# Kernel optimization log

Measured on AMD Instinct MI355X. Metric: run time of the kernel, lower is better.

The kernel has to match this reference:

```python
import jax, jax.numpy as jnp
import numpy as np

N_HEADS = 2

def setup_inputs() -> dict:
    key = jax.random.key(0)
    ks = jax.random.split(key, 10)
    d, bank, b, t = 192, 1000, 16, 4096
    s = 1.0 / np.sqrt(d)
    return {
        "z": jax.random.normal(ks[0], (b, d, t), jnp.float32),
        "memory_bank": jax.random.normal(ks[1], (d, bank), jnp.float32),
        "Wq": jax.random.normal(ks[2], (d, d), jnp.float32) * s,
        "bq": jax.random.normal(ks[3], (d,), jnp.float32) * 0.02,
        "Wk": jax.random.normal(ks[4], (d, d), jnp.float32) * s,
        "bk": jax.random.normal(ks[5], (d,), jnp.float32) * 0.02,
        "Wv": jax.random.normal(ks[6], (d, d), jnp.float32) * s,
        "bv": jax.random.normal(ks[7], (d,), jnp.float32) * 0.02,
        "Wo": jax.random.normal(ks[8], (d, d), jnp.float32) * s,
        "bo": jax.random.normal(ks[9], (d,), jnp.float32) * 0.02,
    }


def _split_heads(x):
    # x: [b, d, t] -> [b, h, t, dk]  (matches view(b, h, dk, t).transpose(2, 3))
    b, d, t = x.shape
    dk = d // N_HEADS
    return x.reshape(b, N_HEADS, dk, t).transpose(0, 1, 3, 2)


def reference(z, memory_bank, Wq, bq, Wk, bk, Wv, bv, Wo, bo):
    b, d, t = z.shape
    dk = d // N_HEADS
    # memory bank expanded over batch: [b, d, bank]
    c = jnp.broadcast_to(memory_bank[None], (b,) + memory_bank.shape)
    # 1x1 conv projections == per-channel linear
    q = jnp.einsum('oc,bct->bot', Wq, z) + bq[None, :, None]
    k = jnp.einsum('oc,bcs->bos', Wk, c) + bk[None, :, None]
    v = jnp.einsum('oc,bcs->bos', Wv, c) + bv[None, :, None]
    qh = _split_heads(q)  # [b, h, t, dk]
    kh = _split_heads(k)  # [b, h, bank, dk]
    vh = _split_heads(v)  # [b, h, bank, dk]
    scores = jnp.einsum('bhtd,bhsd->bhts', qh, kh) / jnp.sqrt(jnp.asarray(dk, z.dtype))
    p = jax.nn.softmax(scores, axis=-1)  # [b, h, t, bank]
    out = jnp.einsum('bhts,bhsd->bhtd', p, vh)  # [b, h, t, dk]
    out = out.transpose(0, 1, 3, 2).reshape(b, d, t)  # merge heads -> [b, d, t]
    return jnp.einsum('oc,bct->bot', Wo, out) + bo[None, :, None]
```

## Files before the change

### kernel.cpp

```cpp
#include <hip/hip_runtime.h>


typedef float  f32x4  __attribute__((ext_vector_type(4)));
typedef __bf16 bf16;
typedef __bf16 bf16x4 __attribute__((ext_vector_type(4)));
typedef __bf16 bf16x8 __attribute__((ext_vector_type(8)));

#define B_   16
#define D_   192
#define T_   4096
#define BANK 1000
#define SP   1024
#define DK   96
#define SCALE 0.10206207261596577f
#define LOG2E 1.4426950408889634f

__global__ __launch_bounds__(256) void kv_kernel(
    const float* __restrict__ mb, const float* __restrict__ Wk, const float* __restrict__ bk,
    const float* __restrict__ Wv, const float* __restrict__ bv,
    bf16* __restrict__ ktg, bf16* __restrict__ vtg) {
  int s = blockIdx.x * 256 + threadIdx.x;
  int o = blockIdx.y;
  int h = o / DK, i = o % DK;
  float ak = 0.f, av = 0.f;
  if (s < BANK) {
    ak = bk[o]; av = bv[o];
    for (int c = 0; c < D_; ++c) {
      float m = mb[c * BANK + s];
      ak += Wk[o * D_ + c] * m;
      av += Wv[o * D_ + c] * m;
    }
  }
  ktg[(size_t)(h * SP + s) * DK + i] = (bf16)ak;
  vtg[(size_t)(h * DK + i) * SP + s] = (bf16)av;
}

__global__ __launch_bounds__(256) void proj_kernel(
    const bf16* __restrict__ XT, const float* __restrict__ W,
    const float* __restrict__ bias, float* __restrict__ Y) {
  __shared__ __align__(16) char smem[24576];
  bf16* sB = (bf16*)smem;
  float* sE = (float*)smem;

  const int tid = threadIdx.x;
  const int t0 = blockIdx.x * 256, o0 = blockIdx.y * 64, b = blockIdx.z;
  const int lane = tid & 63, wv = tid >> 6;
  const int quad = lane >> 4, l15 = lane & 15;

  const bf16* ap[4];
#pragma unroll
  for (int m = 0; m < 4; ++m)
    ap[m] = &XT[((size_t)b * T_ + t0 + (wv * 4 + m) * 16 + l15) * D_ + quad * 8];
  bf16x8 acur[4];
#pragma unroll
  for (int m = 0; m < 4; ++m) acur[m] = *(const bf16x8*)ap[m];

#pragma unroll
  for (int r = 0; r < 6; ++r) {
    int g = tid + 256 * r;
    int kb = g >> 8, nt = (g >> 6) & 3, qd = (g >> 4) & 3, l5 = g & 15;
    const float* wp = &W[(o0 + nt * 16 + l5) * D_ + kb * 32 + qd * 8];
    f32x4 wa = *(const f32x4*)wp, wb = *(const f32x4*)(wp + 4);
    bf16x8 pk;
#pragma unroll
    for (int u = 0; u < 4; ++u) { pk[u] = (bf16)wa[u]; pk[4 + u] = (bf16)wb[u]; }
    *(bf16x8*)&sB[(size_t)g * 8] = pk;
  }

  f32x4 acc[4][4];
#pragma unroll
  for (int m = 0; m < 4; ++m)
#pragma unroll
    for (int n = 0; n < 4; ++n) acc[m][n] = (f32x4){0.f, 0.f, 0.f, 0.f};

  __syncthreads();
  for (int kb = 0; kb < 6; ++kb) {
    bf16x8 anext[4];
    if (kb < 5) {
#pragma unroll
      for (int m = 0; m < 4; ++m)
        anext[m] = *(const bf16x8*)(ap[m] + (kb + 1) * 32);
    }
    bf16x8 bf[4];
#pragma unroll
    for (int n = 0; n < 4; ++n)
      bf[n] = *(const bf16x8*)&sB[(size_t)((kb * 4 + n) * 64 + lane) * 8];
#pragma unroll
    for (int m = 0; m < 4; ++m)
#pragma unroll
      for (int n = 0; n < 4; ++n)
        acc[m][n] = __builtin_amdgcn_mfma_f32_16x16x32_bf16(acur[m], bf[n], acc[m][n], 0, 0, 0);
    if (kb < 5) {
#pragma unroll
      for (int m = 0; m < 4; ++m) acur[m] = anext[m];
    }
  }
  __syncthreads();

  float bs[4];
#pragma unroll
  for (int n = 0; n < 4; ++n) bs[n] = bias[o0 + n * 16 + l15];
  float* se = sE + wv * 1088;
#pragma unroll
  for (int m = 0; m < 4; ++m) {
#pragma unroll
    for (int n = 0; n < 4; ++n)
#pragma unroll
      for (int r = 0; r < 4; ++r)
        se[(quad * 4 + r) * 68 + n * 16 + l15] = acc[m][n][r] + bs[n];
#pragma unroll
    for (int p = 0; p < 4; ++p) {
      int o = p * 16 + (lane >> 2), tq = (lane & 3) * 4;
      f32x4 vv;
#pragma unroll
      for (int u = 0; u < 4; ++u) vv[u] = se[(tq + u) * 68 + o];
      *(f32x4*)&Y[((size_t)b * D_ + o0 + o) * T_ + t0 + wv * 64 + m * 16 + tq] = vv;
    }
  }
}

__global__ __launch_bounds__(512) void attn_kernel(
    const float* __restrict__ z, const float* __restrict__ Wq,
    const float* __restrict__ bq, const bf16* __restrict__ ktg,
    const bf16* __restrict__ vtg, bf16* __restrict__ owsT) {
  __shared__ __align__(16) char smem[32768];
  bf16* kt = (bf16*)smem;
  bf16* vt = (bf16*)(smem + 12288);
  bf16* sP = (bf16*)(smem + 24576);
  bf16* qt = (bf16*)smem;

  const int tid = threadIdx.x;
  const int t0 = blockIdx.x * 128, h = blockIdx.y, b = blockIdx.z;
  const int lane = tid & 63, wv = tid >> 6;
  const int quad = lane >> 4, l15 = lane & 15;

  const bf16* kb_g = ktg + (size_t)h * SP * DK;
  const bf16* vb_g = vtg + (size_t)h * DK * SP;
  const bf16* sp_ptr[3];
  int sp_str[3];
#pragma unroll
  for (int r = 0; r < 3; ++r) {
    int g = tid + 512 * r;
    if (g < 768) {
      int kb = g >> 8, n = (g >> 6) & 3, qd = (g >> 4) & 3, l5 = g & 15;
      sp_ptr[r] = kb_g + (size_t)(n * 16 + l5) * DK + kb * 32 + qd * 8;
      sp_str[r] = 64 * DK;
    } else {
      int gv = g - 768, blk = gv >> 6;
      int kbv = blk / 6, n = blk % 6, qd = (gv >> 4) & 3, l5 = gv & 15;
      sp_ptr[r] = vb_g + (size_t)(n * 16 + l5) * SP + kbv * 32 + qd * 8;
      sp_str[r] = 64;
    }
  }
  bf16x8 kreg[3];
#pragma unroll
  for (int r = 0; r < 3; ++r) kreg[r] = *(const bf16x8*)sp_ptr[r];

  f32x4 qacc[6];
#pragma unroll
  for (int n = 0; n < 6; ++n) qacc[n] = (f32x4){0.f, 0.f, 0.f, 0.f};
  const float* zcol = &z[((size_t)b * D_ + quad * 8) * T_ + t0 + wv * 16 + l15];
  const float* wrow = &Wq[(size_t)(h * DK + l15) * D_ + quad * 8];
  for (int kb = 0; kb < 6; ++kb) {
    bf16x8 zf;
#pragma unroll
    for (int j = 0; j < 8; ++j)
      zf[j] = (bf16)zcol[(size_t)(kb * 32 + j) * T_];
#pragma unroll
    for (int n = 0; n < 6; ++n) {
      const float* wp = wrow + (size_t)n * 16 * D_ + kb * 32;
      f32x4 wa = *(const f32x4*)wp, wb = *(const f32x4*)(wp + 4);
      bf16x8 wf;
#pragma unroll
      for (int u = 0; u < 4; ++u) { wf[u] = (bf16)wa[u]; wf[4 + u] = (bf16)wb[u]; }
      qacc[n] = __builtin_amdgcn_mfma_f32_16x16x32_bf16(wf, zf, qacc[n], 0, 0, 0);
    }
  }
#pragma unroll
  for (int n = 0; n < 6; ++n) {
    f32x4 bq4 = *(const f32x4*)&bq[h * DK + n * 16 + quad * 4];
    int g = ((n & 1) * 2 + (quad >> 1)) * 16 + l15;
    int gs = g ^ ((g >> 3) & 7);
    bf16x4 pk;
#pragma unroll
    for (int r = 0; r < 4; ++r)
      pk[r] = (bf16)((qacc[n][r] + bq4[r]) * (SCALE * LOG2E));
    *(bf16x4*)&qt[(size_t)(((n >> 1) * 8 + wv) * 64 + gs) * 8 + (quad & 1) * 4] = pk;
  }
  bf16x8 qf[3];
#pragma unroll
  for (int kb = 0; kb < 3; ++kb)
    qf[kb] = *(const bf16x8*)&qt[(size_t)((kb * 8 + wv) * 64 + (lane ^ ((lane >> 3) & 7))) * 8];

  f32x4 oaccT[6];
#pragma unroll
  for (int n = 0; n < 6; ++n) oaccT[n] = (f32x4){0.f, 0.f, 0.f, 0.f};
  float m_run = -1e30f, l_run = 0.f;

  for (int ch = 0; ch < 16; ++ch) {
    __syncthreads();
#pragma unroll
    for (int r = 0; r < 3; ++r)
      *(bf16x8*)(smem + (size_t)(tid + 512 * r) * 16) = kreg[r];
    __syncthreads();
    if (ch < 15) {
#pragma unroll
      for (int r = 0; r < 3; ++r) {
        sp_ptr[r] += sp_str[r];
        kreg[r] = *(const bf16x8*)sp_ptr[r];
      }
    }

    f32x4 scT[4];
#pragma unroll
    for (int n = 0; n < 4; ++n) scT[n] = (f32x4){0.f, 0.f, 0.f, 0.f};
#pragma unroll
    for (int kb = 0; kb < 3; ++kb) {
#pragma unroll
      for (int n = 0; n < 4; ++n) {
        bf16x8 kf = *(const bf16x8*)&kt[(size_t)((kb * 4 + n) * 64 + lane) * 8];
        scT[n] = __builtin_amdgcn_mfma_f32_16x16x32_bf16(kf, qf[kb], scT[n], 0, 0, 0);
      }
    }
    if (ch == 15) {
#pragma unroll
      for (int r = 0; r < 4; ++r) {
        scT[3][r] = -1e30f;
        if (quad >= 2) scT[2][r] = -1e30f;
      }
    }

    float m8[8];
#pragma unroll
    for (int u = 0; u < 8; ++u)
      m8[u] = fmaxf(scT[u >> 1][(u & 1) * 2], scT[u >> 1][(u & 1) * 2 + 1]);
    float m4a = fmaxf(m8[0], m8[1]), m4b = fmaxf(m8[2], m8[3]);
    float m4c = fmaxf(m8[4], m8[5]), m4d = fmaxf(m8[6], m8[7]);
    float m0 = fmaxf(fmaxf(m4a, m4b), fmaxf(m4c, m4d));
    m0 = fmaxf(m0, __shfl_xor(m0, 16, 64));
    m0 = fmaxf(m0, __shfl_xor(m0, 32, 64));
    if (!__all(m0 - m_run <= 8.f)) {
      float mn = fmaxf(m_run, m0);
      float al = exp2f(m_run - mn);
      m_run = mn;
      l_run *= al;
#pragma unroll
      for (int n = 0; n < 6; ++n)
#pragma unroll
        for (int r = 0; r < 4; ++r) oaccT[n][r] *= al;
    }
    float pr[4][4];
#pragma unroll
    for (int n = 0; n < 4; ++n)
#pragma unroll
      for (int r = 0; r < 4; ++r) pr[n][r] = exp2f(scT[n][r] - m_run);
    float s8[8];
#pragma unroll
    for (int u = 0; u < 8; ++u)
      s8[u] = pr[u >> 1][(u & 1) * 2] + pr[u >> 1][(u & 1) * 2 + 1];
    float s4a = s8[0] + s8[1], s4b = s8[2] + s8[3];
    float s4c = s8[4] + s8[5], s4d = s8[6] + s8[7];
    float ls = (s4a + s4b) + (s4c + s4d);
    ls += __shfl_xor(ls, 16, 64);
    ls += __shfl_xor(ls, 32, 64);
    l_run += ls;

#pragma unroll
    for (int kb2 = 0; kb2 < 2; ++kb2) {
#pragma unroll
      for (int nh = 0; nh < 2; ++nh) {
        int n = kb2 * 2 + nh;
        int g = (nh * 2 + (quad >> 1)) * 16 + l15;
        int gs = g ^ ((g >> 3) & 7);
        bf16x4 pk = {(bf16)pr[n][0], (bf16)pr[n][1], (bf16)pr[n][2], (bf16)pr[n][3]};
        *(bf16x4*)&sP[(size_t)(wv * 64 + gs) * 8 + (quad & 1) * 4] = pk;
      }
      bf16x8 pa = *(const bf16x8*)&sP[(size_t)(wv * 64 + (lane ^ ((lane >> 3) & 7))) * 8];
#pragma unroll
      for (int n2 = 0; n2 < 6; ++n2) {
        bf16x8 vf = *(const bf16x8*)&vt[(size_t)((kb2 * 6 + n2) * 64 + lane) * 8];
        oaccT[n2] = __builtin_amdgcn_mfma_f32_16x16x32_bf16(vf, pa, oaccT[n2], 0, 0, 0);
      }
    }
  }

  float inv = 1.0f / l_run;
  bf16* orow = &owsT[((size_t)b * T_ + t0 + wv * 16 + l15) * D_ + h * DK + quad * 4];
#pragma unroll
  for (int n2 = 0; n2 < 6; ++n2) {
    bf16x4 pk = {(bf16)(oaccT[n2][0] * inv), (bf16)(oaccT[n2][1] * inv),
                 (bf16)(oaccT[n2][2] * inv), (bf16)(oaccT[n2][3] * inv)};
    *(bf16x4*)&orow[n2 * 16] = pk;
  }
}

extern "C" void kernel_launch(void* const* d_in, const int* in_sizes, int n_in,
                              void* d_out, int out_size, void* d_ws, size_t ws_size,
                              hipStream_t stream) {
  const float* z  = (const float*)d_in[0];
  const float* mb = (const float*)d_in[1];
  const float* Wq = (const float*)d_in[2];
  const float* bq = (const float*)d_in[3];
  const float* Wk = (const float*)d_in[4];
  const float* bk = (const float*)d_in[5];
  const float* Wv = (const float*)d_in[6];
  const float* bv = (const float*)d_in[7];
  const float* Wo = (const float*)d_in[8];
  const float* bo = (const float*)d_in[9];
  float* out = (float*)d_out;

  bf16* ktg  = (bf16*)d_ws;
  bf16* vtg  = ktg + 2 * SP * DK;
  bf16* owsT = vtg + 2 * DK * SP;

  kv_kernel  <<<dim3(SP / 256, D_),    256, 0, stream>>>(mb, Wk, bk, Wv, bv, ktg, vtg);
  attn_kernel<<<dim3(T_ / 128, 2, B_), 512, 0, stream>>>(z, Wq, bq, ktg, vtg, owsT);
  proj_kernel<<<dim3(T_ / 256, 3, B_), 256, 0, stream>>>(owsT, Wo, bo, out);
}
```

Baseline: 257.2 us.

## Process two query tiles per wave in attention kernel with 256 threads

Halves the attention block to 4 waves, with each wave handling two 16-row query tiles instead of one. Each K/V fragment read from shared memory now feeds two MFMAs, which roughly halves LDS reads per unit of work. Each thread also stages twice as many K/V registers from global memory. The cost is higher register pressure (doubled accumulators, 6 prefetch registers) and fewer waves per block for hiding latency. Shared memory grows to 40 KB to hold per-tile P buffers.

```diff
diff --git a/kernel.cpp b/kernel.cpp
--- a/kernel.cpp
+++ b/kernel.cpp
@@ -119,11 +119,11 @@
   }
 }
 
-__global__ __launch_bounds__(512) void attn_kernel(
+__global__ __launch_bounds__(256) void attn_kernel(
     const float* __restrict__ z, const float* __restrict__ Wq,
     const float* __restrict__ bq, const bf16* __restrict__ ktg,
     const bf16* __restrict__ vtg, bf16* __restrict__ owsT) {
-  __shared__ __align__(16) char smem[32768];
+  __shared__ __align__(16) char smem[40960];
   bf16* kt = (bf16*)smem;
   bf16* vt = (bf16*)(smem + 12288);
   bf16* sP = (bf16*)(smem + 24576);
@@ -136,11 +136,11 @@
 
   const bf16* kb_g = ktg + (size_t)h * SP * DK;
   const bf16* vb_g = vtg + (size_t)h * DK * SP;
-  const bf16* sp_ptr[3];
-  int sp_str[3];
-#pragma unroll
-  for (int r = 0; r < 3; ++r) {
-    int g = tid + 512 * r;
+  const bf16* sp_ptr[6];
+  int sp_str[6];
+#pragma unroll
+  for (int r = 0; r < 6; ++r) {
+    int g = tid + 256 * r;
     if (g < 768) {
       int kb = g >> 8, n = (g >> 6) & 3, qd = (g >> 4) & 3, l5 = g & 15;
       sp_ptr[r] = kb_g + (size_t)(n * 16 + l5) * DK + kb * 32 + qd * 8;
@@ -152,20 +152,24 @@
       sp_str[r] = 64;
     }
   }
-  bf16x8 kreg[3];
-#pragma unroll
-  for (int r = 0; r < 3; ++r) kreg[r] = *(const bf16x8*)sp_ptr[r];
-
-  f32x4 qacc[6];
-#pragma unroll
-  for (int n = 0; n < 6; ++n) qacc[n] = (f32x4){0.f, 0.f, 0.f, 0.f};
-  const float* zcol = &z[((size_t)b * D_ + quad * 8) * T_ + t0 + wv * 16 + l15];
+  bf16x8 kreg[6];
+#pragma unroll
+  for (int r = 0; r < 6; ++r) kreg[r] = *(const bf16x8*)sp_ptr[r];
+
+  f32x4 qacc[2][6];
+#pragma unroll
+  for (int t2 = 0; t2 < 2; ++t2)
+#pragma unroll
+    for (int n = 0; n < 6; ++n) qacc[t2][n] = (f32x4){0.f, 0.f, 0.f, 0.f};
+  const float* zc0 = &z[((size_t)b * D_ + quad * 8) * T_ + t0 + wv * 32 + l15];
   const float* wrow = &Wq[(size_t)(h * DK + l15) * D_ + quad * 8];
   for (int kb = 0; kb < 6; ++kb) {
-    bf16x8 zf;
-#pragma unroll
-    for (int j = 0; j < 8; ++j)
-      zf[j] = (bf16)zcol[(size_t)(kb * 32 + j) * T_];
+    bf16x8 zf[2];
+#pragma unroll
+    for (int t2 = 0; t2 < 2; ++t2)
+#pragma unroll
+      for (int j = 0; j < 8; ++j)
+        zf[t2][j] = (bf16)zc0[(size_t)(kb * 32 + j) * T_ + t2 * 16];
 #pragma unroll
     for (int n = 0; n < 6; ++n) {
       const float* wp = wrow + (size_t)n * 16 * D_ + kb * 32;
@@ -173,124 +177,158 @@
       bf16x8 wf;
 #pragma unroll
       for (int u = 0; u < 4; ++u) { wf[u] = (bf16)wa[u]; wf[4 + u] = (bf16)wb[u]; }
-      qacc[n] = __builtin_amdgcn_mfma_f32_16x16x32_bf16(wf, zf, qacc[n], 0, 0, 0);
-    }
-  }
-#pragma unroll
-  for (int n = 0; n < 6; ++n) {
-    f32x4 bq4 = *(const f32x4*)&bq[h * DK + n * 16 + quad * 4];
-    int g = ((n & 1) * 2 + (quad >> 1)) * 16 + l15;
-    int gs = g ^ ((g >> 3) & 7);
-    bf16x4 pk;
-#pragma unroll
-    for (int r = 0; r < 4; ++r)
-      pk[r] = (bf16)((qacc[n][r] + bq4[r]) * (SCALE * LOG2E));
-    *(bf16x4*)&qt[(size_t)(((n >> 1) * 8 + wv) * 64 + gs) * 8 + (quad & 1) * 4] = pk;
-  }
-  bf16x8 qf[3];
-#pragma unroll
-  for (int kb = 0; kb < 3; ++kb)
-    qf[kb] = *(const bf16x8*)&qt[(size_t)((kb * 8 + wv) * 64 + (lane ^ ((lane >> 3) & 7))) * 8];
-
-  f32x4 oaccT[6];
-#pragma unroll
-  for (int n = 0; n < 6; ++n) oaccT[n] = (f32x4){0.f, 0.f, 0.f, 0.f};
-  float m_run = -1e30f, l_run = 0.f;
+      qacc[0][n] = __builtin_amdgcn_mfma_f32_16x16x32_bf16(wf, zf[0], qacc[0][n], 0, 0, 0);
+      qacc[1][n] = __builtin_amdgcn_mfma_f32_16x16x32_bf16(wf, zf[1], qacc[1][n], 0, 0, 0);
+    }
+  }
+#pragma unroll
+  for (int t2 = 0; t2 < 2; ++t2)
+#pragma unroll
+    for (int n = 0; n < 6; ++n) {
+      f32x4 bq4 = *(const f32x4*)&bq[h * DK + n * 16 + quad * 4];
+      int g = ((n & 1) * 2 + (quad >> 1)) * 16 + l15;
+      int gs = g ^ ((g >> 3) & 7);
+      bf16x4 pk;
+#pragma unroll
+      for (int r = 0; r < 4; ++r)
+        pk[r] = (bf16)((qacc[t2][n][r] + bq4[r]) * (SCALE * LOG2E));
+      *(bf16x4*)&qt[(size_t)(((n >> 1) * 8 + wv * 2 + t2) * 64 + gs) * 8 + (quad & 1) * 4] = pk;
+    }
+  bf16x8 qf[2][3];
+#pragma unroll
+  for (int t2 = 0; t2 < 2; ++t2)
+#pragma unroll
+    for (int kb = 0; kb < 3; ++kb)
+      qf[t2][kb] = *(const bf16x8*)&qt[(size_t)((kb * 8 + wv * 2 + t2) * 64 +
+                                                (lane ^ ((lane >> 3) & 7))) * 8];
+
+  f32x4 oaccT[2][6];
+#pragma unroll
+  for (int t2 = 0; t2 < 2; ++t2)
+#pragma unroll
+    for (int n = 0; n < 6; ++n) oaccT[t2][n] = (f32x4){0.f, 0.f, 0.f, 0.f};
+  float m_run[2] = {-1e30f, -1e30f}, l_run[2] = {0.f, 0.f};
 
   for (int ch = 0; ch < 16; ++ch) {
     __syncthreads();
 #pragma unroll
-    for (int r = 0; r < 3; ++r)
-      *(bf16x8*)(smem + (size_t)(tid + 512 * r) * 16) = kreg[r];
+    for (int r = 0; r < 6; ++r)
+      *(bf16x8*)(smem + (size_t)(tid + 256 * r) * 16) = kreg[r];
     __syncthreads();
     if (ch < 15) {
 #pragma unroll
-      for (int r = 0; r < 3; ++r) {
+      for (int r = 0; r < 6; ++r) {
         sp_ptr[r] += sp_str[r];
         kreg[r] = *(const bf16x8*)sp_ptr[r];
       }
     }
 
-    f32x4 scT[4];
-#pragma unroll
-    for (int n = 0; n < 4; ++n) scT[n] = (f32x4){0.f, 0.f, 0.f, 0.f};
+    f32x4 scT[2][4];
+#pragma unroll
+    for (int t2 = 0; t2 < 2; ++t2)
+#pragma unroll
+      for (int n = 0; n < 4; ++n) scT[t2][n] = (f32x4){0.f, 0.f, 0.f, 0.f};
 #pragma unroll
     for (int kb = 0; kb < 3; ++kb) {
 #pragma unroll
       for (int n = 0; n < 4; ++n) {
         bf16x8 kf = *(const bf16x8*)&kt[(size_t)((kb * 4 + n) * 64 + lane) * 8];
-        scT[n] = __builtin_amdgcn_mfma_f32_16x16x32_bf16(kf, qf[kb], scT[n], 0, 0, 0);
+        scT[0][n] = __builtin_amdgcn_mfma_f32_16x16x32_bf16(kf, qf[0][kb], scT[0][n], 0, 0, 0);
+        scT[1][n] = __builtin_amdgcn_mfma_f32_16x16x32_bf16(kf, qf[1][kb], scT[1][n], 0, 0, 0);
       }
     }
     if (ch == 15) {
 #pragma unroll
-      for (int r = 0; r < 4; ++r) {
-        scT[3][r] = -1e30f;
-        if (quad >= 2) scT[2][r] = -1e30f;
+      for (int t2 = 0; t2 < 2; ++t2)
+#pragma unroll
+        for (int r = 0; r < 4; ++r) {
+          scT[t2][3][r] = -1e30f;
+          if (quad >= 2) scT[t2][2][r] = -1e30f;
+        }
+    }
+
+    float mt[2];
+#pragma unroll
+    for (int t2 = 0; t2 < 2; ++t2) {
+      float m8[8];
+#pragma unroll
+      for (int u = 0; u < 8; ++u)
+        m8[u] = fmaxf(scT[t2][u >> 1][(u & 1) * 2], scT[t2][u >> 1][(u & 1) * 2 + 1]);
+      float ma = fmaxf(fmaxf(m8[0], m8[1]), fmaxf(m8[2], m8[3]));
+      float mb2 = fmaxf(fmaxf(m8[4], m8[5]), fmaxf(m8[6], m8[7]));
+      float m0 = fmaxf(ma, mb2);
+      m0 = fmaxf(m0, __shfl_xor(m0, 16, 64));
+      m0 = fmaxf(m0, __shfl_xor(m0, 32, 64));
+      mt[t2] = m0;
+    }
+    if (!__all(mt[0] - m_run[0] <= 8.f && mt[1] - m_run[1] <= 8.f)) {
+#pragma unroll
+      for (int t2 = 0; t2 < 2; ++t2) {
+        float mn = fmaxf(m_run[t2], mt[t2]);
+        float al = exp2f(m_run[t2] - mn);
+        m_run[t2] = mn;
+        l_run[t2] *= al;
+#pragma unroll
+        for (int n = 0; n < 6; ++n)
+#pragma unroll
+          for (int r = 0; r < 4; ++r) oaccT[t2][n][r] *= al;
       }
     }
-
-    float m8[8];
-#pragma unroll
-    for (int u = 0; u < 8; ++u)
-      m8[u] = fmaxf(scT[u >> 1][(u & 1) * 2], scT[u >> 1][(u & 1) * 2 + 1]);
-    float m4a = fmaxf(m8[0], m8[1]), m4b = fmaxf(m8[2], m8[3]);
-    float m4c = fmaxf(m8[4], m8[5]), m4d = fmaxf(m8[6], m8[7]);
-    float m0 = fmaxf(fmaxf(m4a, m4b), fmaxf(m4c, m4d));
-    m0 = fmaxf(m0, __shfl_xor(m0, 16, 64));
-    m0 = fmaxf(m0, __shfl_xor(m0, 32, 64));
-    if (!__all(m0 - m_run <= 8.f)) {
-      float mn = fmaxf(m_run, m0);
-      float al = exp2f(m_run - mn);
-      m_run = mn;
-      l_run *= al;
-#pragma unroll
-      for (int n = 0; n < 6; ++n)
-#pragma unroll
-        for (int r = 0; r < 4; ++r) oaccT[n][r] *= al;
-    }
-    float pr[4][4];
-#pragma unroll
-    for (int n = 0; n < 4; ++n)
-#pragma unroll
-      for (int r = 0; r < 4; ++r) pr[n][r] = exp2f(scT[n][r] - m_run);
-    float s8[8];
-#pragma unroll
-    for (int u = 0; u < 8; ++u)
-      s8[u] = pr[u >> 1][(u & 1) * 2] + pr[u >> 1][(u & 1) * 2 + 1];
-    float s4a = s8[0] + s8[1], s4b = s8[2] + s8[3];
-    float s4c = s8[4] + s8[5], s4d = s8[6] + s8[7];
-    float ls = (s4a + s4b) + (s4c + s4d);
-    ls += __shfl_xor(ls, 16, 64);
-    ls += __shfl_xor(ls, 32, 64);
-    l_run += ls;
+#pragma unroll
+    for (int t2 = 0; t2 < 2; ++t2) {
+      float pr[4][4];
+#pragma unroll
+      for (int n = 0; n < 4; ++n)
+#pragma unroll
+        for (int r = 0; r < 4; ++r) pr[n][r] = exp2f(scT[t2][n][r] - m_run[t2]);
+      float s8[8];
+#pragma unroll
+      for (int u = 0; u < 8; ++u)
+        s8[u] = pr[u >> 1][(u & 1) * 2] + pr[u >> 1][(u & 1) * 2 + 1];
+      float ls = ((s8[0] + s8[1]) + (s8[2] + s8[3])) + ((s8[4] + s8[5]) + (s8[6] + s8[7]));
+      ls += __shfl_xor(ls, 16, 64);
+      ls += __shfl_xor(ls, 32, 64);
+      l_run[t2] += ls;
+#pragma unroll
+      for (int kb2 = 0; kb2 < 2; ++kb2)
+#pragma unroll
+        for (int nh = 0; nh < 2; ++nh) {
+          int n = kb2 * 2 + nh;
+          int g = (nh * 2 + (quad >> 1)) * 16 + l15;
+          int gs = g ^ ((g >> 3) & 7);
+          bf16x4 pk = {(bf16)pr[n][0], (bf16)pr[n][1], (bf16)pr[n][2], (bf16)pr[n][3]};
+          *(bf16x4*)&sP[(size_t)(((wv * 2 + t2) * 2 + kb2) * 64 + gs) * 8 +
+                        (quad & 1) * 4] = pk;
+        }
+    }
 
 #pragma unroll
     for (int kb2 = 0; kb2 < 2; ++kb2) {
-#pragma unroll
-      for (int nh = 0; nh < 2; ++nh) {
-        int n = kb2 * 2 + nh;
-        int g = (nh * 2 + (quad >> 1)) * 16 + l15;
-        int gs = g ^ ((g >> 3) & 7);
-        bf16x4 pk = {(bf16)pr[n][0], (bf16)pr[n][1], (bf16)pr[n][2], (bf16)pr[n][3]};
-        *(bf16x4*)&sP[(size_t)(wv * 64 + gs) * 8 + (quad & 1) * 4] = pk;
-      }
-      bf16x8 pa = *(const bf16x8*)&sP[(size_t)(wv * 64 + (lane ^ ((lane >> 3) & 7))) * 8];
+      bf16x8 pa[2];
+#pragma unroll
+      for (int t2 = 0; t2 < 2; ++t2)
+        pa[t2] = *(const bf16x8*)&sP[(size_t)(((wv * 2 + t2) * 2 + kb2) * 64 +
+                                              (lane ^ ((lane >> 3) & 7))) * 8];
 #pragma unroll
       for (int n2 = 0; n2 < 6; ++n2) {
         bf16x8 vf = *(const bf16x8*)&vt[(size_t)((kb2 * 6 + n2) * 64 + lane) * 8];
-        oaccT[n2] = __builtin_amdgcn_mfma_f32_16x16x32_bf16(vf, pa, oaccT[n2], 0, 0, 0);
+        oaccT[0][n2] = __builtin_amdgcn_mfma_f32_16x16x32_bf16(vf, pa[0], oaccT[0][n2], 0, 0, 0);
+        oaccT[1][n2] = __builtin_amdgcn_mfma_f32_16x16x32_bf16(vf, pa[1], oaccT[1][n2], 0, 0, 0);
       }
     }
   }
 
-  float inv = 1.0f / l_run;
-  bf16* orow = &owsT[((size_t)b * T_ + t0 + wv * 16 + l15) * D_ + h * DK + quad * 4];
-#pragma unroll
-  for (int n2 = 0; n2 < 6; ++n2) {
-    bf16x4 pk = {(bf16)(oaccT[n2][0] * inv), (bf16)(oaccT[n2][1] * inv),
-                 (bf16)(oaccT[n2][2] * inv), (bf16)(oaccT[n2][3] * inv)};
-    *(bf16x4*)&orow[n2 * 16] = pk;
+#pragma unroll
+  for (int t2 = 0; t2 < 2; ++t2) {
+    float inv = 1.0f / l_run[t2];
+    bf16* orow = &owsT[((size_t)b * T_ + t0 + wv * 32 + t2 * 16 + l15) * D_ +
+                       h * DK + quad * 4];
+#pragma unroll
+    for (int n2 = 0; n2 < 6; ++n2) {
+      bf16x4 pk = {(bf16)(oaccT[t2][n2][0] * inv), (bf16)(oaccT[t2][n2][1] * inv),
+                   (bf16)(oaccT[t2][n2][2] * inv), (bf16)(oaccT[t2][n2][3] * inv)};
+      *(bf16x4*)&orow[n2 * 16] = pk;
+    }
   }
 }
 
@@ -314,6 +352,6 @@
   bf16* owsT = vtg + 2 * DK * SP;
 
   kv_kernel  <<<dim3(SP / 256, D_),    256, 0, stream>>>(mb, Wk, bk, Wv, bv, ktg, vtg);
-  attn_kernel<<<dim3(T_ / 128, 2, B_), 512, 0, stream>>>(z, Wq, bq, ktg, vtg, owsT);
+  attn_kernel<<<dim3(T_ / 128, 2, B_), 256, 0, stream>>>(z, Wq, bq, ktg, vtg, owsT);
   proj_kernel<<<dim3(T_ / 256, 3, B_), 256, 0, stream>>>(owsT, Wo, bo, out);
 }
```

Result: faster. 245.2 us (-4.7%).
